# Performance work log

Hardware: AMD Instinct MI355X
Metric: run time of the kernel (lower is better)

The kernel has to match this reference:

```python
import jax, jax.numpy as jnp
import numpy as np

NEG_INF = -1e30  # stand-in for float('-inf') that is fp16/bf16-safe


def setup_inputs() -> dict:
    key = jax.random.key(0)
    ks = jax.random.split(key, 6)
    B, S, D, E = 4, 4096, 2048, 64
    return {
        "x": jax.random.normal(ks[0], (B, S, D), dtype=jnp.float32),
        "router_w": jax.random.normal(ks[1], (E, D), dtype=jnp.float32) * (1.0 / np.sqrt(D)),
        "router_b": jax.random.normal(ks[2], (E,), dtype=jnp.float32) * 0.01,
        "noise_w": jax.random.normal(ks[3], (E, D), dtype=jnp.float32) * (1.0 / np.sqrt(D)),
        "noise_b": jax.random.normal(ks[4], (E,), dtype=jnp.float32) * 0.01,
        "noise_u": jax.random.uniform(ks[5], (B, S, E), dtype=jnp.float32),
        "top_k": 2,
    }


def reference(x, router_w, router_b, noise_w, noise_b, noise_u, top_k):
    E = router_w.shape[0]
    # dual linear projections: [B,S,D] x [D,E] -> [B,S,E]
    logits = jnp.einsum("bsd,ed->bse", x, router_w) + router_b
    noise_scale = jax.nn.softplus(jnp.einsum("bsd,ed->bse", x, noise_w) + noise_b)
    noisy = logits + noise_scale * noise_u  # noise_u plays role of torch.rand_like
    # top-k over experts
    max_k, max_k_index = jax.lax.top_k(noisy, top_k)  # [B,S,k]
    # scatter top-k values into -inf-filled tensor == keep noisy at topk slots
    keep = jnp.sum(jax.nn.one_hot(max_k_index, E, dtype=noisy.dtype), axis=-2) > 0  # [B,S,E]
    sparse = jnp.where(keep, noisy, NEG_INF)
    sf_sparse_topk = jax.nn.softmax(sparse, axis=-1)
    return (sf_sparse_topk, max_k_index)
```

## Files before the change

kernel.cpp:

```cpp
#include <hip/hip_runtime.h>
#include <math.h>

typedef __fp16   fp16x2  __attribute__((ext_vector_type(2)));
typedef _Float16 half8   __attribute__((ext_vector_type(8)));
typedef float    floatx4 __attribute__((ext_vector_type(4)));

#define M_TOTAL 16384
#define K_DIM   2048
#define NCOL    128
#define BM      32
#define BK      32
#define NT      256
#define NCHUNK  (K_DIM / BK)

#define A_HI  0
#define A_LO  1024
#define B_HI  2048
#define B_LO  6144
#define BUF_H 10240

__device__ __forceinline__ void gl_lds16(const _Float16* g, _Float16* l) {
    __builtin_amdgcn_global_load_lds((const __attribute__((address_space(1))) void*)g,
                                     (__attribute__((address_space(3))) void*)l, 16, 0, 0);
}

__device__ __forceinline__ void cvt_store(const float4 v, _Float16* hiP, _Float16* loP) {
    fp16x2 h01 = __builtin_amdgcn_cvt_pkrtz(v.x, v.y);
    fp16x2 h23 = __builtin_amdgcn_cvt_pkrtz(v.z, v.w);
    float r0 = (v.x - (float)h01.x) * 2048.0f;
    float r1 = (v.y - (float)h01.y) * 2048.0f;
    float r2 = (v.z - (float)h23.x) * 2048.0f;
    float r3 = (v.w - (float)h23.y) * 2048.0f;
    fp16x2 l01 = __builtin_amdgcn_cvt_pkrtz(r0, r1);
    fp16x2 l23 = __builtin_amdgcn_cvt_pkrtz(r2, r3);
    union { fp16x2 h[2]; uint2 u; } ph, pl;
    ph.h[0] = h01; ph.h[1] = h23;
    pl.h[0] = l01; pl.h[1] = l23;
    *(uint2*)hiP = ph.u;
    *(uint2*)loP = pl.u;
}

__global__ __launch_bounds__(256) void conv_w_kernel(
    const float* __restrict__ rw, const float* __restrict__ nw,
    _Float16* __restrict__ wsB)
{
    const int u   = blockIdx.x * 256 + threadIdx.x;
    const int col = u & 127;
    const int g   = (u >> 7) & 3;
    const int c   = u >> 9;
    const float* srcRow = (col < 64) ? (rw + (size_t)col * K_DIM)
                                     : (nw + (size_t)(col - 64) * K_DIM);
    const float* src = srcRow + c * BK + g * 8;
    const float4 v0 = *(const float4*)src;
    const float4 v1 = *(const float4*)(src + 4);
    union { fp16x2 h[4]; uint4 q; } ph, pl;
    ph.h[0] = __builtin_amdgcn_cvt_pkrtz(v0.x, v0.y);
    ph.h[1] = __builtin_amdgcn_cvt_pkrtz(v0.z, v0.w);
    ph.h[2] = __builtin_amdgcn_cvt_pkrtz(v1.x, v1.y);
    ph.h[3] = __builtin_amdgcn_cvt_pkrtz(v1.z, v1.w);
    pl.h[0] = __builtin_amdgcn_cvt_pkrtz((v0.x - (float)ph.h[0].x) * 2048.0f,
                                         (v0.y - (float)ph.h[0].y) * 2048.0f);
    pl.h[1] = __builtin_amdgcn_cvt_pkrtz((v0.z - (float)ph.h[1].x) * 2048.0f,
                                         (v0.w - (float)ph.h[1].y) * 2048.0f);
    pl.h[2] = __builtin_amdgcn_cvt_pkrtz((v1.x - (float)ph.h[2].x) * 2048.0f,
                                         (v1.y - (float)ph.h[2].y) * 2048.0f);
    pl.h[3] = __builtin_amdgcn_cvt_pkrtz((v1.z - (float)ph.h[3].x) * 2048.0f,
                                         (v1.w - (float)ph.h[3].y) * 2048.0f);
    const size_t base = (size_t)c * 8192 + ((size_t)g * 128 + col) * 8;
    *(uint4*)&wsB[base]        = ph.q;
    *(uint4*)&wsB[base + 4096] = pl.q;
}

__global__ __launch_bounds__(NT, 2) void gemm_router_kernel(
    const float* __restrict__ x,
    const _Float16* __restrict__ wsB,
    const float* __restrict__ router_b,
    const float* __restrict__ noise_b,
    const float* __restrict__ noise_u,
    float* __restrict__ out)
{
    __shared__ __align__(16) union {
        _Float16 S[2 * BUF_H];
        struct { float Cs[32][132]; float p1[32]; float p2[32]; int i1[32]; int i2[32]; } e;
    } sm;

    const int t    = threadIdx.x;
    const int lane = t & 63;
    const int w    = t >> 6;
    const int rowBase = blockIdx.x * BM;

    const int r = t >> 3, q = t & 7;
    const float* pa = x + (size_t)(rowBase + r) * K_DIM + q * 4;
    const int aw = ((q >> 1) * 32 + r) * 8 + (q & 1) * 4;

    const int lr  = lane & 15;
    const int lg4 = lane >> 4;
    const int mt0 = (w & 1) * 16;
    const int nt0 = (w >> 1) * 64;
    const int aOff = (lg4 * 32 + mt0 + lr) * 8;

    floatx4 acch[4], accx[4];
    #pragma unroll
    for (int ni = 0; ni < 4; ++ni) { acch[ni] = (floatx4)0.0f; accx[ni] = (floatx4)0.0f; }

    float4 aReg = *(const float4*)pa;
    {
        #pragma unroll
        for (int i = 0; i < 4; ++i) {
            const int n = w * 4 + i;
            gl_lds16(wsB + n * 512 + lane * 8, &sm.S[B_HI + n * 512]);
        }
    }
    cvt_store(aReg, &sm.S[A_HI + aw], &sm.S[A_LO + aw]);

    for (int c = 0; c < NCHUNK; ++c) {
        __syncthreads();
        _Float16* buf  = sm.S + (c & 1) * BUF_H;
        _Float16* bufn = sm.S + ((c + 1) & 1) * BUF_H;

        if (c + 1 < NCHUNK) {
            const _Float16* wc = wsB + (size_t)(c + 1) * 8192;
            #pragma unroll
            for (int i = 0; i < 4; ++i) {
                const int n = w * 4 + i;
                gl_lds16(wc + n * 512 + lane * 8, bufn + B_HI + n * 512);
            }
            aReg = *(const float4*)(pa + (c + 1) * BK);
        }

        const half8 ah = *(const half8*)&buf[A_HI + aOff];
        const half8 al = *(const half8*)&buf[A_LO + aOff];
        half8 bh[4], bl[4];
        #pragma unroll
        for (int ni = 0; ni < 4; ++ni) {
            const int bo = (lg4 * 128 + nt0 + ni * 16 + lr) * 8;
            bh[ni] = *(const half8*)&buf[B_HI + bo];
            bl[ni] = *(const half8*)&buf[B_LO + bo];
        }
        #pragma unroll
        for (int ni = 0; ni < 4; ++ni) {
            acch[ni] = __builtin_amdgcn_mfma_f32_16x16x32_f16(ah, bh[ni], acch[ni], 0, 0, 0);
            accx[ni] = __builtin_amdgcn_mfma_f32_16x16x32_f16(ah, bl[ni], accx[ni], 0, 0, 0);
            accx[ni] = __builtin_amdgcn_mfma_f32_16x16x32_f16(al, bh[ni], accx[ni], 0, 0, 0);
        }
        if (c + 1 < NCHUNK)
            cvt_store(aReg, &bufn[A_HI + aw], &bufn[A_LO + aw]);
    }

    #pragma unroll
    for (int ni = 0; ni < 4; ++ni) {
        const floatx4 v = acch[ni] + accx[ni] * (1.0f / 2048.0f);
        const int col = nt0 + ni * 16 + lr;
        #pragma unroll
        for (int reg = 0; reg < 4; ++reg)
            sm.e.Cs[mt0 + lg4 * 4 + reg][col] = v[reg];
    }
    __syncthreads();

    {
        const int sr = t >> 3;
        const int eg = (t & 7) * 8;
        const int grow = rowBase + sr;
        const float* urow = noise_u + (size_t)grow * 64 + eg;
        const float4 u0 = *(const float4*)urow;
        const float4 u1 = *(const float4*)(urow + 4);
        const float uu[8] = {u0.x, u0.y, u0.z, u0.w, u1.x, u1.y, u1.z, u1.w};
        float v1 = -3.0e38f, v2 = -3.0e38f;
        int i1 = 0, i2 = 0;
        #pragma unroll
        for (int j = 0; j < 8; ++j) {
            const int e = eg + j;
            const float lg = sm.e.Cs[sr][e] + router_b[e];
            const float nz = sm.e.Cs[sr][64 + e] + noise_b[e];
            const float sp = fmaxf(nz, 0.0f) + log1pf(expf(-fabsf(nz)));
            const float nv = lg + sp * uu[j];
            if (nv > v1)      { v2 = v1; i2 = i1; v1 = nv; i1 = e; }
            else if (nv > v2) { v2 = nv; i2 = e; }
        }
        #pragma unroll
        for (int m = 1; m < 8; m <<= 1) {
            const float ov1 = __shfl_xor(v1, m, 64);
            const int   oi1 = __shfl_xor(i1, m, 64);
            const float ov2 = __shfl_xor(v2, m, 64);
            const int   oi2 = __shfl_xor(i2, m, 64);
            const bool takeO = (ov1 > v1) || (ov1 == v1 && oi1 < i1);
            const float t1v = takeO ? ov1 : v1;  const int t1i = takeO ? oi1 : i1;
            const float c2v = takeO ? v1 : ov1;  const int c2i = takeO ? i1 : oi1;
            const float c3v = takeO ? ov2 : v2;  const int c3i = takeO ? oi2 : i2;
            const bool k2 = (c3v > c2v) || (c3v == c2v && c3i < c2i);
            v1 = t1v; i1 = t1i;
            v2 = k2 ? c3v : c2v; i2 = k2 ? c3i : c2i;
        }
        if ((t & 7) == 0) {
            const float e2 = expf(v2 - v1);
            const float dn = 1.0f + e2;
            sm.e.p1[sr] = 1.0f / dn;
            sm.e.p2[sr] = e2 / dn;
            sm.e.i1[sr] = i1;
            sm.e.i2[sr] = i2;
            float2 idx2;
            idx2.x = (float)i1;
            idx2.y = (float)i2;
            *(float2*)&out[(size_t)M_TOTAL * 64 + (size_t)grow * 2] = idx2;
        }
    }
    __syncthreads();

    {
        const int rr = t >> 3;
        const int e0 = (t & 7) * 8;
        const int g2 = rowBase + rr;
        const int j1 = sm.e.i1[rr], j2 = sm.e.i2[rr];
        const float q1 = sm.e.p1[rr], q2 = sm.e.p2[rr];
        float* orow = out + (size_t)g2 * 64;
        #pragma unroll
        for (int g = 0; g < 2; ++g) {
            const int b0 = e0 + g * 4;
            float4 v;
            v.x = (b0 + 0 == j1) ? q1 : (b0 + 0 == j2) ? q2 : 0.0f;
            v.y = (b0 + 1 == j1) ? q1 : (b0 + 1 == j2) ? q2 : 0.0f;
            v.z = (b0 + 2 == j1) ? q1 : (b0 + 2 == j2) ? q2 : 0.0f;
            v.w = (b0 + 3 == j1) ? q1 : (b0 + 3 == j2) ? q2 : 0.0f;
            *(float4*)&orow[b0] = v;
        }
    }
}

extern "C" void kernel_launch(void* const* d_in, const int* in_sizes, int n_in,
                              void* d_out, int out_size, void* d_ws, size_t ws_size,
                              hipStream_t stream) {
    const float* x  = (const float*)d_in[0];
    const float* rw = (const float*)d_in[1];
    const float* rb = (const float*)d_in[2];
    const float* nw = (const float*)d_in[3];
    const float* nb = (const float*)d_in[4];
    const float* nu = (const float*)d_in[5];
    float* out = (float*)d_out;
    _Float16* wsB = (_Float16*)d_ws;
    (void)in_sizes; (void)n_in; (void)out_size; (void)ws_size;

    hipLaunchKernelGGL(conv_w_kernel, dim3(128), dim3(256), 0, stream, rw, nw, wsB);
    hipLaunchKernelGGL(gemm_router_kernel, dim3(M_TOTAL / BM), dim3(NT), 0, stream,
                       x, wsB, rb, nb, nu, out);
}
```

Baseline: 237.8 us.

## Load GEMM fragments directly from global into registers, drop LDS staging

The main loop no longer stages x and the split-fp16 weights through shared memory with per-chunk barriers. Each lane now loads its own MFMA A and B fragments straight from global memory into registers, double-buffered two chunks ahead, and converts A to hi/lo fp16 in registers. This removes the LDS round trip and the __syncthreads per K chunk. In exchange, weight fragments are reloaded redundantly by the waves that share them, global accesses are less coalesced (each lane reads 32 bytes of its own row), and register pressure rises.

```diff
diff --git a/kernel.cpp b/kernel.cpp
--- a/kernel.cpp
+++ b/kernel.cpp
@@ -7,38 +7,10 @@
 
 #define M_TOTAL 16384
 #define K_DIM   2048
-#define NCOL    128
 #define BM      32
 #define BK      32
 #define NT      256
 #define NCHUNK  (K_DIM / BK)
-
-#define A_HI  0
-#define A_LO  1024
-#define B_HI  2048
-#define B_LO  6144
-#define BUF_H 10240
-
-__device__ __forceinline__ void gl_lds16(const _Float16* g, _Float16* l) {
-    __builtin_amdgcn_global_load_lds((const __attribute__((address_space(1))) void*)g,
-                                     (__attribute__((address_space(3))) void*)l, 16, 0, 0);
-}
-
-__device__ __forceinline__ void cvt_store(const float4 v, _Float16* hiP, _Float16* loP) {
-    fp16x2 h01 = __builtin_amdgcn_cvt_pkrtz(v.x, v.y);
-    fp16x2 h23 = __builtin_amdgcn_cvt_pkrtz(v.z, v.w);
-    float r0 = (v.x - (float)h01.x) * 2048.0f;
-    float r1 = (v.y - (float)h01.y) * 2048.0f;
-    float r2 = (v.z - (float)h23.x) * 2048.0f;
-    float r3 = (v.w - (float)h23.y) * 2048.0f;
-    fp16x2 l01 = __builtin_amdgcn_cvt_pkrtz(r0, r1);
-    fp16x2 l23 = __builtin_amdgcn_cvt_pkrtz(r2, r3);
-    union { fp16x2 h[2]; uint2 u; } ph, pl;
-    ph.h[0] = h01; ph.h[1] = h23;
-    pl.h[0] = l01; pl.h[1] = l23;
-    *(uint2*)hiP = ph.u;
-    *(uint2*)loP = pl.u;
-}
 
 __global__ __launch_bounds__(256) void conv_w_kernel(
     const float* __restrict__ rw, const float* __restrict__ nw,
@@ -71,6 +43,25 @@
     *(uint4*)&wsB[base + 4096] = pl.q;
 }
 
+__device__ __forceinline__ void cvt_frag(const float4 v0, const float4 v1,
+                                         half8* ah, half8* al) {
+    union { fp16x2 h[4]; half8 v; } uh, ul;
+    uh.h[0] = __builtin_amdgcn_cvt_pkrtz(v0.x, v0.y);
+    uh.h[1] = __builtin_amdgcn_cvt_pkrtz(v0.z, v0.w);
+    uh.h[2] = __builtin_amdgcn_cvt_pkrtz(v1.x, v1.y);
+    uh.h[3] = __builtin_amdgcn_cvt_pkrtz(v1.z, v1.w);
+    ul.h[0] = __builtin_amdgcn_cvt_pkrtz((v0.x - (float)uh.h[0].x) * 2048.0f,
+                                         (v0.y - (float)uh.h[0].y) * 2048.0f);
+    ul.h[1] = __builtin_amdgcn_cvt_pkrtz((v0.z - (float)uh.h[1].x) * 2048.0f,
+                                         (v0.w - (float)uh.h[1].y) * 2048.0f);
+    ul.h[2] = __builtin_amdgcn_cvt_pkrtz((v1.x - (float)uh.h[2].x) * 2048.0f,
+                                         (v1.y - (float)uh.h[2].y) * 2048.0f);
+    ul.h[3] = __builtin_amdgcn_cvt_pkrtz((v1.z - (float)uh.h[3].x) * 2048.0f,
+                                         (v1.w - (float)uh.h[3].y) * 2048.0f);
+    *ah = uh.v;
+    *al = ul.v;
+}
+
 __global__ __launch_bounds__(NT, 2) void gemm_router_kernel(
     const float* __restrict__ x,
     const _Float16* __restrict__ wsB,
@@ -79,9 +70,9 @@
     const float* __restrict__ noise_u,
     float* __restrict__ out)
 {
-    __shared__ __align__(16) union {
-        _Float16 S[2 * BUF_H];
-        struct { float Cs[32][132]; float p1[32]; float p2[32]; int i1[32]; int i2[32]; } e;
+    __shared__ struct {
+        float Cs[32][132];
+        float p1[32]; float p2[32]; int i1[32]; int i2[32];
     } sm;
 
     const int t    = threadIdx.x;
@@ -89,62 +80,64 @@
     const int w    = t >> 6;
     const int rowBase = blockIdx.x * BM;
 
-    const int r = t >> 3, q = t & 7;
-    const float* pa = x + (size_t)(rowBase + r) * K_DIM + q * 4;
-    const int aw = ((q >> 1) * 32 + r) * 8 + (q & 1) * 4;
-
     const int lr  = lane & 15;
     const int lg4 = lane >> 4;
     const int mt0 = (w & 1) * 16;
     const int nt0 = (w >> 1) * 64;
-    const int aOff = (lg4 * 32 + mt0 + lr) * 8;
+
+    const float* pa = x + (size_t)(rowBase + mt0 + lr) * K_DIM + lg4 * 8;
+    const _Float16* pbh[4];
+    #pragma unroll
+    for (int ni = 0; ni < 4; ++ni)
+        pbh[ni] = wsB + ((size_t)lg4 * 128 + nt0 + ni * 16 + lr) * 8;
 
     floatx4 acch[4], accx[4];
     #pragma unroll
     for (int ni = 0; ni < 4; ++ni) { acch[ni] = (floatx4)0.0f; accx[ni] = (floatx4)0.0f; }
 
-    float4 aReg = *(const float4*)pa;
-    {
-        #pragma unroll
-        for (int i = 0; i < 4; ++i) {
-            const int n = w * 4 + i;
-            gl_lds16(wsB + n * 512 + lane * 8, &sm.S[B_HI + n * 512]);
-        }
-    }
-    cvt_store(aReg, &sm.S[A_HI + aw], &sm.S[A_LO + aw]);
+    float4 a0s[2], a1s[2];
+    uint4  bhs[2][4], bls[2][4];
+
+    #pragma unroll
+    for (int s = 0; s < 2; ++s) {
+        a0s[s] = *(const float4*)(pa + s * BK);
+        a1s[s] = *(const float4*)(pa + s * BK + 4);
+        #pragma unroll
+        for (int ni = 0; ni < 4; ++ni) {
+            bhs[s][ni] = *(const uint4*)(pbh[ni] + (size_t)s * 8192);
+            bls[s][ni] = *(const uint4*)(pbh[ni] + (size_t)s * 8192 + 4096);
+        }
+    }
 
     for (int c = 0; c < NCHUNK; ++c) {
-        __syncthreads();
-        _Float16* buf  = sm.S + (c & 1) * BUF_H;
-        _Float16* bufn = sm.S + ((c + 1) & 1) * BUF_H;
-
-        if (c + 1 < NCHUNK) {
-            const _Float16* wc = wsB + (size_t)(c + 1) * 8192;
+        const int s = c & 1;
+
+        half8 ah, al;
+        cvt_frag(a0s[s], a1s[s], &ah, &al);
+        half8 bh[4], bl[4];
+        #pragma unroll
+        for (int ni = 0; ni < 4; ++ni) {
+            union { uint4 q; half8 v; } cb;
+            cb.q = bhs[s][ni]; bh[ni] = cb.v;
+            cb.q = bls[s][ni]; bl[ni] = cb.v;
+        }
+
+        if (c + 2 < NCHUNK) {
+            a0s[s] = *(const float4*)(pa + (c + 2) * BK);
+            a1s[s] = *(const float4*)(pa + (c + 2) * BK + 4);
             #pragma unroll
-            for (int i = 0; i < 4; ++i) {
-                const int n = w * 4 + i;
-                gl_lds16(wc + n * 512 + lane * 8, bufn + B_HI + n * 512);
+            for (int ni = 0; ni < 4; ++ni) {
+                bhs[s][ni] = *(const uint4*)(pbh[ni] + (size_t)(c + 2) * 8192);
+                bls[s][ni] = *(const uint4*)(pbh[ni] + (size_t)(c + 2) * 8192 + 4096);
             }
-            aReg = *(const float4*)(pa + (c + 1) * BK);
-        }
-
-        const half8 ah = *(const half8*)&buf[A_HI + aOff];
-        const half8 al = *(const half8*)&buf[A_LO + aOff];
-        half8 bh[4], bl[4];
-        #pragma unroll
-        for (int ni = 0; ni < 4; ++ni) {
-            const int bo = (lg4 * 128 + nt0 + ni * 16 + lr) * 8;
-            bh[ni] = *(const half8*)&buf[B_HI + bo];
-            bl[ni] = *(const half8*)&buf[B_LO + bo];
-        }
+        }
+
         #pragma unroll
         for (int ni = 0; ni < 4; ++ni) {
             acch[ni] = __builtin_amdgcn_mfma_f32_16x16x32_f16(ah, bh[ni], acch[ni], 0, 0, 0);
             accx[ni] = __builtin_amdgcn_mfma_f32_16x16x32_f16(ah, bl[ni], accx[ni], 0, 0, 0);
             accx[ni] = __builtin_amdgcn_mfma_f32_16x16x32_f16(al, bh[ni], accx[ni], 0, 0, 0);
         }
-        if (c + 1 < NCHUNK)
-            cvt_store(aReg, &bufn[A_HI + aw], &bufn[A_LO + aw]);
     }
 
     #pragma unroll
@@ -153,7 +146,7 @@
         const int col = nt0 + ni * 16 + lr;
         #pragma unroll
         for (int reg = 0; reg < 4; ++reg)
-            sm.e.Cs[mt0 + lg4 * 4 + reg][col] = v[reg];
+            sm.Cs[mt0 + lg4 * 4 + reg][col] = v[reg];
     }
     __syncthreads();
 
@@ -170,8 +163,8 @@
         #pragma unroll
         for (int j = 0; j < 8; ++j) {
             const int e = eg + j;
-            const float lg = sm.e.Cs[sr][e] + router_b[e];
-            const float nz = sm.e.Cs[sr][64 + e] + noise_b[e];
+            const float lg = sm.Cs[sr][e] + router_b[e];
+            const float nz = sm.Cs[sr][64 + e] + noise_b[e];
             const float sp = fmaxf(nz, 0.0f) + log1pf(expf(-fabsf(nz)));
             const float nv = lg + sp * uu[j];
             if (nv > v1)      { v2 = v1; i2 = i1; v1 = nv; i1 = e; }
@@ -194,10 +187,10 @@
         if ((t & 7) == 0) {
             const float e2 = expf(v2 - v1);
             const float dn = 1.0f + e2;
-            sm.e.p1[sr] = 1.0f / dn;
-            sm.e.p2[sr] = e2 / dn;
-            sm.e.i1[sr] = i1;
-            sm.e.i2[sr] = i2;
+            sm.p1[sr] = 1.0f / dn;
+            sm.p2[sr] = e2 / dn;
+            sm.i1[sr] = i1;
+            sm.i2[sr] = i2;
             float2 idx2;
             idx2.x = (float)i1;
             idx2.y = (float)i2;
@@ -210,8 +203,8 @@
         const int rr = t >> 3;
         const int e0 = (t & 7) * 8;
         const int g2 = rowBase + rr;
-        const int j1 = sm.e.i1[rr], j2 = sm.e.i2[rr];
-        const float q1 = sm.e.p1[rr], q2 = sm.e.p2[rr];
+        const int j1 = sm.i1[rr], j2 = sm.i2[rr];
+        const float q1 = sm.p1[rr], q2 = sm.p2[rr];
         float* orow = out + (size_t)g2 * 64;
         #pragma unroll
         for (int g = 0; g < 2; ++g) {
```

New measurement: 767.2 us. 223% more time.
